# Optimization experiments

Measured on AMD Instinct MI355X. Metric: run time of the kernel, lower is better.

The kernel has to match this reference:

```python
import jax, jax.numpy as jnp
import numpy as np

B, H, S, D = 2, 16, 2048, 64
SCALE = D ** -0.5  # head_dim^-0.5 with dim=1024, num_heads=16


def setup_inputs() -> dict:
    key = jax.random.key(0)
    kq, kk, kv = jax.random.split(key, 3)
    q = jax.random.normal(kq, (B, H, S, D), dtype=jnp.float32)
    k = jax.random.normal(kk, (B, H, S, D), dtype=jnp.float32)
    v = jax.random.normal(kv, (B, H, S, D), dtype=jnp.float32)
    # causal mask, broadcastable over batch and heads; 0 -> masked
    mask = jnp.tril(jnp.ones((S, S), dtype=jnp.int32))[None, None]
    return {"q": q, "k": k, "v": v, "mask": mask}


def reference(q, k, v, mask):
    # scores: [B, H, S, S]
    scores = jnp.einsum("bhqd,bhkd->bhqk", q, k) * SCALE
    scores = jnp.where(mask == 0, jnp.float32(-jnp.inf), scores)
    attn_weights = jax.nn.softmax(scores, axis=-1)
    # dropout p=0 / eval mode -> identity
    attn_output = jnp.einsum("bhqk,bhkd->bhqd", attn_weights, v)
    return attn_output, attn_weights
```

## Files before the change

### kernel.cpp

```cpp
#include <hip/hip_runtime.h>


#define S_LEN 2048
#define HD 64
#define NHEADS 32
#define NQT 32
#define ATT_SCALE 0.125f

typedef __bf16 bf16x8 __attribute__((ext_vector_type(8)));
typedef unsigned short u16x8 __attribute__((ext_vector_type(8)));
typedef float f32x4 __attribute__((ext_vector_type(4)));

__device__ __forceinline__ unsigned short f2bf(float f) {
  unsigned int u = __builtin_bit_cast(unsigned int, f);
  u += 0x7fffu + ((u >> 16) & 1u);
  return (unsigned short)(u >> 16);
}
__device__ __forceinline__ bf16x8 frag16(const unsigned short* p) {
  uint4 u = *reinterpret_cast<const uint4*>(p);
  return __builtin_bit_cast(bf16x8, u);
}
__device__ __forceinline__ bf16x8 cvt8(const float* p) {
  const float4 a = *reinterpret_cast<const float4*>(p);
  const float4 b = *reinterpret_cast<const float4*>(p + 4);
  u16x8 r;
  r[0] = f2bf(a.x); r[1] = f2bf(a.y); r[2] = f2bf(a.z); r[3] = f2bf(a.w);
  r[4] = f2bf(b.x); r[5] = f2bf(b.y); r[6] = f2bf(b.z); r[7] = f2bf(b.w);
  return __builtin_bit_cast(bf16x8, r);
}
__device__ __forceinline__ bf16x8 load8(const void* base, size_t off, bool isf32) {
  if (isf32) return cvt8(reinterpret_cast<const float*>(base) + off);
  return frag16(reinterpret_cast<const unsigned short*>(base) + off);
}
__device__ __forceinline__ bool sniff_f32(const void* q) {
  const int lane = threadIdx.x & 63;
  const unsigned int w = reinterpret_cast<const unsigned int*>(q)[lane];
  const unsigned int le = (w >> 7) & 0xFFu;
  const bool okb = (le == 0u) || (le >= 100u && le <= 140u);
  return __popcll(__ballot(okb)) < 32;
}
__device__ __forceinline__ int swz3(int r) { return (r & 3) | (((r >> 3) & 1) << 2); }

__global__ __launch_bounds__(256) void prep_kernel(
    const void* __restrict__ q, const void* __restrict__ k, const void* __restrict__ v,
    unsigned short* __restrict__ wq, unsigned short* __restrict__ wk,
    unsigned short* __restrict__ wv) {
  __shared__ __align__(16) unsigned short T[HD][72];
  const int tid = threadIdx.x;
  if (blockIdx.x >= 1024) {
    const bool isf32 = sniff_f32(q);
    const size_t i = ((size_t)(blockIdx.x - 1024) * 256 + tid) * 8;
    bf16x8 a = load8(q, i, isf32);
    *reinterpret_cast<uint4*>(wq + i) = __builtin_bit_cast(uint4, a);
    bf16x8 b = load8(k, i, isf32);
    const int d0 = (int)(i & 63);
    const int t = (int)((i >> 6) & (S_LEN - 1));
    const int head = (int)(i >> 17);
    const int tl = t & 63;
    const int sch = (d0 >> 3) ^ swz3(tl);
    unsigned short* dst =
        wk + (((size_t)(head << 5) + (t >> 6)) << 12) + tl * 64 + (sch << 3);
    *reinterpret_cast<uint4*>(dst) = __builtin_bit_cast(uint4, b);
    return;
  }
  const bool isf32 = sniff_f32(v);
  const int head = blockIdx.x & (NHEADS - 1);
  const int tt = blockIdx.x >> 5;
  const int r = tid >> 2;
  const int dc = (tid & 3) << 4;
  const size_t off = ((size_t)head * S_LEN + (tt << 6) + r) * HD + dc;
  const bf16x8 x0 = load8(v, off, isf32);
  const bf16x8 x1 = load8(v, off + 8, isf32);
  const u16x8 e0 = __builtin_bit_cast(u16x8, x0);
  const u16x8 e1 = __builtin_bit_cast(u16x8, x1);
#pragma unroll
  for (int e = 0; e < 8; ++e) { T[dc + e][r] = e0[e]; T[dc + 8 + e][r] = e1[e]; }
  __syncthreads();
  const int d = tid >> 2;
  const int tc = (tid & 3) << 4;
  const int c0 = tc >> 3;
  unsigned short* base = wv + (((size_t)(head << 5) + tt) << 12) + d * 64;
  *reinterpret_cast<uint4*>(base + ((c0 ^ swz3(d)) << 3)) =
      *reinterpret_cast<const uint4*>(&T[d][tc]);
  *reinterpret_cast<uint4*>(base + (((c0 + 1) ^ swz3(d)) << 3)) =
      *reinterpret_cast<const uint4*>(&T[d][tc + 8]);
}

__global__ __launch_bounds__(256, 4) void attn_ws(
    const unsigned short* __restrict__ wq, const unsigned short* __restrict__ wk,
    const unsigned short* __restrict__ wv,
    float* __restrict__ out_o, float* __restrict__ out_w) {
  __shared__ __align__(16) unsigned short Kl[2][4096];
  __shared__ __align__(16) unsigned short Vl[2][4096];

  const int blk = blockIdx.x;
  const int head = blk & (NHEADS - 1);
  const int qt = (NQT - 1) - (blk >> 5);
  const int tid = threadIdx.x;
  const int lane = tid & 63;
  const int wave = tid >> 6;
  const int q0 = qt << 6;
  const int r0 = q0 + (wave << 4);
  const int l15 = lane & 15;
  const int quad = lane >> 4;
  const int kswz = (l15 & 3) | (((l15 >> 2) & 1) << 2);
  const int vswz = (l15 & 3) | (((l15 >> 3) & 1) << 2);
  const int krow_l = ((l15 >> 2) << 3) + (l15 & 3);
  const int qi = r0 + l15;

  float* Wh = out_w + (size_t)head * S_LEN * S_LEN;
  const unsigned short* wkh = wk + ((size_t)head << 17);
  const unsigned short* wvh = wv + ((size_t)head << 17);

  const size_t qoff = ((size_t)head << 17) + (size_t)(r0 + l15) * HD + (quad << 3);
  const bf16x8 qa0 = frag16(wq + qoff);
  const bf16x8 qa1 = frag16(wq + qoff + 32);

  const int so = wave * 1024 + lane * 8;
  uint4 sk0, sk1, sv0, sv1;
  auto ldKg = [&](int kt) {
    const unsigned short* p = wkh + ((size_t)kt << 12) + so;
    sk0 = *reinterpret_cast<const uint4*>(p);
    sk1 = *reinterpret_cast<const uint4*>(p + 512);
  };
  auto wrK = [&](int b) {
    unsigned short* p = &Kl[b][so];
    *reinterpret_cast<uint4*>(p) = sk0;
    *reinterpret_cast<uint4*>(p + 512) = sk1;
  };
  auto ldVg = [&](int kt) {
    const unsigned short* p = wvh + ((size_t)kt << 12) + so;
    sv0 = *reinterpret_cast<const uint4*>(p);
    sv1 = *reinterpret_cast<const uint4*>(p + 512);
  };
  auto wrV = [&](int b) {
    unsigned short* p = &Vl[b][so];
    *reinterpret_cast<uint4*>(p) = sv0;
    *reinterpret_cast<uint4*>(p + 512) = sv1;
  };

  float lsum = 0.f;
  ldKg(0); wrK(0); __syncthreads();
  for (int kt = 0; kt <= qt; ++kt) {
    if (kt < qt) ldKg(kt + 1);
    const unsigned short* Kb = &Kl[kt & 1][0];
#pragma unroll
    for (int s = 0; s < 4; ++s) {
      const int R = krow_l + ((s & 1) << 2) + ((s >> 1) << 5);
      const unsigned short* rb = Kb + R * 64;
      const bf16x8 k0 = frag16(rb + ((quad ^ kswz) << 3));
      const bf16x8 k1 = frag16(rb + (((4 + quad) ^ kswz) << 3));
      f32x4 acc = {0.f, 0.f, 0.f, 0.f};
      acc = __builtin_amdgcn_mfma_f32_16x16x32_bf16(k0, qa0, acc, 0, 0, 0);
      acc = __builtin_amdgcn_mfma_f32_16x16x32_bf16(k1, qa1, acc, 0, 0, 0);
      if (kt == qt) {
        const int kib = (kt << 6) + (quad << 3) + ((s & 1) << 2) + ((s >> 1) << 5);
#pragma unroll
        for (int r = 0; r < 4; ++r)
          lsum += (kib + r <= qi) ? __expf(acc[r] * ATT_SCALE) : 0.f;
      } else {
#pragma unroll
        for (int r = 0; r < 4; ++r) lsum += __expf(acc[r] * ATT_SCALE);
      }
    }
    if (kt < qt) { wrK((kt + 1) & 1); __syncthreads(); }
  }
  lsum += __shfl_xor(lsum, 16);
  lsum += __shfl_xor(lsum, 32);
  const float inv_l = 1.0f / lsum;
  __syncthreads();

  const f32x4 vz = {0.f, 0.f, 0.f, 0.f};
  f32x4 oacc[4] = {vz, vz, vz, vz};
  ldKg(0); ldVg(0); wrK(0); wrV(0); __syncthreads();
  for (int kt = 0; kt <= qt; ++kt) {
    const bool last = (kt == qt);
    if (!last) { ldKg(kt + 1); ldVg(kt + 1); }
    const unsigned short* Kb = &Kl[kt & 1][0];
    const unsigned short* Vb = &Vl[kt & 1][0];

    float pb[4][4];
#pragma unroll
    for (int s = 0; s < 4; ++s) {
      const int R = krow_l + ((s & 1) << 2) + ((s >> 1) << 5);
      const unsigned short* rb = Kb + R * 64;
      const bf16x8 k0 = frag16(rb + ((quad ^ kswz) << 3));
      const bf16x8 k1 = frag16(rb + (((4 + quad) ^ kswz) << 3));
      f32x4 acc = {0.f, 0.f, 0.f, 0.f};
      acc = __builtin_amdgcn_mfma_f32_16x16x32_bf16(k0, qa0, acc, 0, 0, 0);
      acc = __builtin_amdgcn_mfma_f32_16x16x32_bf16(k1, qa1, acc, 0, 0, 0);
      const int kib = (kt << 6) + (quad << 3) + ((s & 1) << 2) + ((s >> 1) << 5);
      f32x4 pv;
#pragma unroll
      for (int r = 0; r < 4; ++r) {
        float p = __expf(acc[r] * ATT_SCALE) * inv_l;
        if (last) p = (kib + r <= qi) ? p : 0.f;
        pb[s][r] = p;
        pv[r] = p;
      }
      *reinterpret_cast<f32x4*>(Wh + (size_t)qi * S_LEN + kib) = pv;
    }
    u16x8 a0, a1;
#pragma unroll
    for (int r = 0; r < 4; ++r) {
      a0[r] = f2bf(pb[0][r]); a0[4 + r] = f2bf(pb[1][r]);
      a1[r] = f2bf(pb[2][r]); a1[4 + r] = f2bf(pb[3][r]);
    }
    const bf16x8 pa0 = __builtin_bit_cast(bf16x8, a0);
    const bf16x8 pa1 = __builtin_bit_cast(bf16x8, a1);
#pragma unroll
    for (int nc2 = 0; nc2 < 4; ++nc2) {
      const unsigned short* rb = Vb + ((nc2 << 4) + l15) * 64;
      const bf16x8 v0 = frag16(rb + ((quad ^ vswz) << 3));
      const bf16x8 v1 = frag16(rb + (((4 + quad) ^ vswz) << 3));
      oacc[nc2] = __builtin_amdgcn_mfma_f32_16x16x32_bf16(pa0, v0, oacc[nc2], 0, 0, 0);
      oacc[nc2] = __builtin_amdgcn_mfma_f32_16x16x32_bf16(pa1, v1, oacc[nc2], 0, 0, 0);
    }
    if (!last) { wrK((kt + 1) & 1); wrV((kt + 1) & 1); __syncthreads(); }
  }

#pragma unroll
  for (int nc2 = 0; nc2 < 4; ++nc2)
#pragma unroll
    for (int r = 0; r < 4; ++r)
      out_o[(size_t)(head * S_LEN + r0 + (quad << 2) + r) * HD + (nc2 << 4) + l15] =
          oacc[nc2][r];

  {
    const int c0 = (qt + 1) << 6;
    const f32x4 z = {0.f, 0.f, 0.f, 0.f};
#pragma unroll 1
    for (int rr = 0; rr < 16; ++rr) {
      float* rowp = Wh + (size_t)(r0 + rr) * S_LEN;
      for (int c = c0 + (lane << 2); c < S_LEN; c += 256)
        __builtin_nontemporal_store(z, reinterpret_cast<f32x4*>(rowp + c));
    }
  }
}

__global__ __launch_bounds__(256, 4) void attn_fb(
    const void* __restrict__ q, const void* __restrict__ kk, const void* __restrict__ vv,
    float* __restrict__ out_o, float* __restrict__ out_w) {
  __shared__ __align__(16) unsigned short Vt[2 * HD * 72];

  const int blk = blockIdx.x;
  const int head = blk & (NHEADS - 1);
  const int qt = (NQT - 1) - (blk >> 5);
  const int tid = threadIdx.x;
  const int lane = tid & 63;
  const int wave = tid >> 6;
  const int q0 = qt << 6;
  const int r0 = q0 + (wave << 4);
  const int l15 = lane & 15;
  const int quad = lane >> 4;
  const bool isf32 = sniff_f32(q);

  const size_t qb = (size_t)head * S_LEN * HD;
  float* Wh = out_w + (size_t)head * S_LEN * S_LEN;

  {
    const int c0 = (qt + 1) << 6;
    const int nz4 = (S_LEN - c0) >> 2;
    const int row = tid >> 2;
    const f32x4 z = {0.f, 0.f, 0.f, 0.f};
    f32x4* wrow = reinterpret_cast<f32x4*>(Wh + (size_t)(q0 + row) * S_LEN + c0);
    for (int c = tid & 3; c < nz4; c += 4) wrow[c] = z;
  }

  const size_t qoff = qb + (size_t)(r0 + l15) * HD + (quad << 3);
  const bf16x8 qa0 = load8(q, qoff, isf32);
  const bf16x8 qa1 = load8(q, qoff + 32, isf32);

  const int krow_l = ((l15 >> 2) << 3) + (l15 & 3);
  auto ldk = [&](int kt, int f) -> bf16x8 {
    const int s = f >> 1;
    const int row = (kt << 6) + krow_l + ((s & 1) << 2) + ((s >> 1) << 5);
    const size_t o = qb + (size_t)row * HD + (quad << 3) + ((f & 1) << 5);
    return load8(kk, o, isf32);
  };
  const int kib_base = (quad << 3);
  const int qi = r0 + l15;

  float lsum = 0.f;
  {
    bf16x8 kc[8], kn[8];
#pragma unroll
    for (int f = 0; f < 8; ++f) kc[f] = ldk(0, f);
    for (int kt = 0; kt <= qt; ++kt) {
      if (kt < qt) {
#pragma unroll
        for (int f = 0; f < 8; ++f) kn[f] = ldk(kt + 1, f);
      }
#pragma unroll
      for (int s = 0; s < 4; ++s) {
        f32x4 acc = {0.f, 0.f, 0.f, 0.f};
        acc = __builtin_amdgcn_mfma_f32_16x16x32_bf16(kc[2 * s], qa0, acc, 0, 0, 0);
        acc = __builtin_amdgcn_mfma_f32_16x16x32_bf16(kc[2 * s + 1], qa1, acc, 0, 0, 0);
        const int kib = (kt << 6) + kib_base + ((s & 1) << 2) + ((s >> 1) << 5);
#pragma unroll
        for (int r = 0; r < 4; ++r)
          lsum += (kt < qt || kib + r <= qi) ? __expf(acc[r] * ATT_SCALE) : 0.f;
      }
      if (kt < qt) {
#pragma unroll
        for (int f = 0; f < 8; ++f) kc[f] = kn[f];
      }
    }
  }
  lsum += __shfl_xor(lsum, 16);
  lsum += __shfl_xor(lsum, 32);
  const float inv_l = 1.0f / lsum;

  const f32x4 vz = {0.f, 0.f, 0.f, 0.f};
  f32x4 oacc[4] = {vz, vz, vz, vz};

  const int ftr1 = tid >> 3, fdc = (tid & 7) << 3;
  const int ftr2 = (tid + 256) >> 3;
  bf16x8 fv0, fv1;
  auto vload = [&](int kt) {
    fv0 = load8(vv, qb + (size_t)((kt << 6) + ftr1) * HD + fdc, isf32);
    fv1 = load8(vv, qb + (size_t)((kt << 6) + ftr2) * HD + fdc, isf32);
  };
  auto vstage = [&](int buf) {
    const u16x8 s0 = __builtin_bit_cast(u16x8, fv0);
    const u16x8 s1 = __builtin_bit_cast(u16x8, fv1);
    const int tb1 = ftr1 >> 3, tl1 = ftr1 & 7;
    const int tb2 = ftr2 >> 3, tl2 = ftr2 & 7;
    unsigned short* Vb = &Vt[buf * HD * 72];
#pragma unroll
    for (int e = 0; e < 8; ++e) {
      const int d = fdc + e;
      Vb[d * 72 + (((tb1 ^ (d >> 3)) << 3) | tl1)] = s0[e];
      Vb[d * 72 + (((tb2 ^ (d >> 3)) << 3) | tl2)] = s1[e];
    }
  };
  vload(0);
  vstage(0);
  __syncthreads();
  for (int kt = 0; kt <= qt; ++kt) {
    const bool last = (kt == qt);
    bf16x8 kf[8];
#pragma unroll
    for (int f = 0; f < 8; ++f) kf[f] = ldk(kt, f);
    if (!last) vload(kt + 1);

    float pb[4][4];
#pragma unroll
    for (int s = 0; s < 4; ++s) {
      f32x4 acc = {0.f, 0.f, 0.f, 0.f};
      acc = __builtin_amdgcn_mfma_f32_16x16x32_bf16(kf[2 * s], qa0, acc, 0, 0, 0);
      acc = __builtin_amdgcn_mfma_f32_16x16x32_bf16(kf[2 * s + 1], qa1, acc, 0, 0, 0);
      const int kib = (kt << 6) + kib_base + ((s & 1) << 2) + ((s >> 1) << 5);
      f32x4 pv;
#pragma unroll
      for (int r = 0; r < 4; ++r) {
        float p = __expf(acc[r] * ATT_SCALE) * inv_l;
        if (last) p = (kib + r <= qi) ? p : 0.f;
        pb[s][r] = p;
        pv[r] = p;
      }
      *reinterpret_cast<f32x4*>(Wh + (size_t)qi * S_LEN + kib) = pv;
    }
    u16x8 a0, a1;
#pragma unroll
    for (int r = 0; r < 4; ++r) {
      a0[r] = f2bf(pb[0][r]); a0[4 + r] = f2bf(pb[1][r]);
      a1[r] = f2bf(pb[2][r]); a1[4 + r] = f2bf(pb[3][r]);
    }
    const bf16x8 pa0 = __builtin_bit_cast(bf16x8, a0);
    const bf16x8 pa1 = __builtin_bit_cast(bf16x8, a1);
    const unsigned short* Vc = &Vt[(kt & 1) * HD * 72];
#pragma unroll
    for (int nc2 = 0; nc2 < 4; ++nc2) {
      const int n = (nc2 << 4) + l15;
      const unsigned short* vbp = Vc + n * 72;
      const int nb = n >> 3;
      const bf16x8 v0 = frag16(vbp + ((quad ^ nb) << 3));
      const bf16x8 v1 = frag16(vbp + (((4 + quad) ^ nb) << 3));
      oacc[nc2] = __builtin_amdgcn_mfma_f32_16x16x32_bf16(pa0, v0, oacc[nc2], 0, 0, 0);
      oacc[nc2] = __builtin_amdgcn_mfma_f32_16x16x32_bf16(pa1, v1, oacc[nc2], 0, 0, 0);
    }
    if (!last) {
      vstage((kt + 1) & 1);
      __syncthreads();
    }
  }

#pragma unroll
  for (int nc2 = 0; nc2 < 4; ++nc2)
#pragma unroll
    for (int r = 0; r < 4; ++r)
      out_o[(size_t)(head * S_LEN + r0 + (quad << 2) + r) * HD + (nc2 << 4) + l15] =
          oacc[nc2][r];
}

extern "C" void kernel_launch(void* const* d_in, const int* in_sizes, int n_in,
                              void* d_out, int out_size, void* d_ws, size_t ws_size,
                              hipStream_t stream) {
  (void)in_sizes; (void)n_in; (void)out_size;
  const void* q = d_in[0];
  const void* k = d_in[1];
  const void* v = d_in[2];
  float* out = (float*)d_out;
  float* out_o = out;
  float* out_w = out + (size_t)NHEADS * S_LEN * HD;
  const size_t NE = (size_t)NHEADS * S_LEN * HD;
  if (d_ws && ws_size >= NE * 2 * 3) {
    unsigned short* wq = reinterpret_cast<unsigned short*>(d_ws);
    unsigned short* wk = wq + NE;
    unsigned short* wv = wk + NE;
    prep_kernel<<<dim3(1024 + NE / (256 * 8)), dim3(256), 0, stream>>>(q, k, v, wq, wk, wv);
    attn_ws<<<dim3(NHEADS * NQT), dim3(256), 0, stream>>>(wq, wk, wv, out_o, out_w);
  } else {
    attn_fb<<<dim3(NHEADS * NQT), dim3(256), 0, stream>>>(q, k, v, out_o, out_w);
  }
}
```

Measured before the change: 634.4 us.

## Double query rows per block, pair causal tiles, and map heads to XCDs

Each block now handles 128 query rows, with each wave computing two 16-row groups, so every K/V tile loaded into shared memory serves twice as many rows. The grid is cut to 512 blocks. Block indices are remapped so each XCD handles four heads, which keeps K/V reads for a head within one L2. Query tiles are ordered so long and short causal tiles are interleaved to balance load. The costs are more registers (launch bounds lowered to 2 blocks per SIMD), fewer blocks in flight, and some wasted work on the masked half of the diagonal tiles.

```diff
diff --git a/kernel.cpp b/kernel.cpp
--- a/kernel.cpp
+++ b/kernel.cpp
@@ -86,35 +86,44 @@
       *reinterpret_cast<const uint4*>(&T[d][tc + 8]);
 }
 
-__global__ __launch_bounds__(256, 4) void attn_ws(
+__global__ __launch_bounds__(256, 2) void attn_ws(
     const unsigned short* __restrict__ wq, const unsigned short* __restrict__ wk,
     const unsigned short* __restrict__ wv,
     float* __restrict__ out_o, float* __restrict__ out_w) {
   __shared__ __align__(16) unsigned short Kl[2][4096];
   __shared__ __align__(16) unsigned short Vl[2][4096];
 
-  const int blk = blockIdx.x;
-  const int head = blk & (NHEADS - 1);
-  const int qt = (NQT - 1) - (blk >> 5);
+  const int b = blockIdx.x;
+  const int xcd = b & 7;
+  const int slot = b >> 3;
+  const int head = (xcd << 2) + (slot & 3);
+  const int u = slot >> 2;
+  const int jj = (u < 8) ? u : (23 - u);
+  const int qthi = 2 * jj + 1;
+  const int q0 = jj << 7;
+
   const int tid = threadIdx.x;
   const int lane = tid & 63;
   const int wave = tid >> 6;
-  const int q0 = qt << 6;
-  const int r0 = q0 + (wave << 4);
   const int l15 = lane & 15;
   const int quad = lane >> 4;
   const int kswz = (l15 & 3) | (((l15 >> 2) & 1) << 2);
   const int vswz = (l15 & 3) | (((l15 >> 3) & 1) << 2);
   const int krow_l = ((l15 >> 2) << 3) + (l15 & 3);
-  const int qi = r0 + l15;
+  const int rg0 = q0 + (wave << 5);
+  const int rg1 = rg0 + 16;
+  const int qi0 = rg0 + l15;
+  const int qi1 = rg1 + l15;
 
   float* Wh = out_w + (size_t)head * S_LEN * S_LEN;
   const unsigned short* wkh = wk + ((size_t)head << 17);
   const unsigned short* wvh = wv + ((size_t)head << 17);
 
-  const size_t qoff = ((size_t)head << 17) + (size_t)(r0 + l15) * HD + (quad << 3);
-  const bf16x8 qa0 = frag16(wq + qoff);
-  const bf16x8 qa1 = frag16(wq + qoff + 32);
+  const size_t hq = (size_t)head << 17;
+  const bf16x8 qa00 = frag16(wq + hq + (size_t)qi0 * HD + (quad << 3));
+  const bf16x8 qa01 = frag16(wq + hq + (size_t)qi0 * HD + (quad << 3) + 32);
+  const bf16x8 qa10 = frag16(wq + hq + (size_t)qi1 * HD + (quad << 3));
+  const bf16x8 qa11 = frag16(wq + hq + (size_t)qi1 * HD + (quad << 3) + 32);
 
   const int so = wave * 1024 + lane * 8;
   uint4 sk0, sk1, sv0, sv1;
@@ -123,8 +132,8 @@
     sk0 = *reinterpret_cast<const uint4*>(p);
     sk1 = *reinterpret_cast<const uint4*>(p + 512);
   };
-  auto wrK = [&](int b) {
-    unsigned short* p = &Kl[b][so];
+  auto wrK = [&](int bb) {
+    unsigned short* p = &Kl[bb][so];
     *reinterpret_cast<uint4*>(p) = sk0;
     *reinterpret_cast<uint4*>(p + 512) = sk1;
   };
@@ -133,88 +142,122 @@
     sv0 = *reinterpret_cast<const uint4*>(p);
     sv1 = *reinterpret_cast<const uint4*>(p + 512);
   };
-  auto wrV = [&](int b) {
-    unsigned short* p = &Vl[b][so];
+  auto wrV = [&](int bb) {
+    unsigned short* p = &Vl[bb][so];
     *reinterpret_cast<uint4*>(p) = sv0;
     *reinterpret_cast<uint4*>(p + 512) = sv1;
   };
 
-  float lsum = 0.f;
+  float ls0 = 0.f, ls1 = 0.f;
   ldKg(0); wrK(0); __syncthreads();
-  for (int kt = 0; kt <= qt; ++kt) {
-    if (kt < qt) ldKg(kt + 1);
+  for (int kt = 0; kt <= qthi; ++kt) {
+    if (kt < qthi) ldKg(kt + 1);
     const unsigned short* Kb = &Kl[kt & 1][0];
+    const int kb6 = kt << 6;
+    const bool m0 = kb6 + 63 > rg0;
+    const bool m1 = kb6 + 63 > rg1;
 #pragma unroll
     for (int s = 0; s < 4; ++s) {
       const int R = krow_l + ((s & 1) << 2) + ((s >> 1) << 5);
       const unsigned short* rb = Kb + R * 64;
       const bf16x8 k0 = frag16(rb + ((quad ^ kswz) << 3));
       const bf16x8 k1 = frag16(rb + (((4 + quad) ^ kswz) << 3));
-      f32x4 acc = {0.f, 0.f, 0.f, 0.f};
-      acc = __builtin_amdgcn_mfma_f32_16x16x32_bf16(k0, qa0, acc, 0, 0, 0);
-      acc = __builtin_amdgcn_mfma_f32_16x16x32_bf16(k1, qa1, acc, 0, 0, 0);
-      if (kt == qt) {
-        const int kib = (kt << 6) + (quad << 3) + ((s & 1) << 2) + ((s >> 1) << 5);
+      const int kib = kb6 + (quad << 3) + ((s & 1) << 2) + ((s >> 1) << 5);
+      f32x4 a0 = {0.f, 0.f, 0.f, 0.f};
+      a0 = __builtin_amdgcn_mfma_f32_16x16x32_bf16(k0, qa00, a0, 0, 0, 0);
+      a0 = __builtin_amdgcn_mfma_f32_16x16x32_bf16(k1, qa01, a0, 0, 0, 0);
+      f32x4 a1 = {0.f, 0.f, 0.f, 0.f};
+      a1 = __builtin_amdgcn_mfma_f32_16x16x32_bf16(k0, qa10, a1, 0, 0, 0);
+      a1 = __builtin_amdgcn_mfma_f32_16x16x32_bf16(k1, qa11, a1, 0, 0, 0);
+      if (m0) {
 #pragma unroll
         for (int r = 0; r < 4; ++r)
-          lsum += (kib + r <= qi) ? __expf(acc[r] * ATT_SCALE) : 0.f;
+          ls0 += (kib + r <= qi0) ? __expf(a0[r] * ATT_SCALE) : 0.f;
       } else {
 #pragma unroll
-        for (int r = 0; r < 4; ++r) lsum += __expf(acc[r] * ATT_SCALE);
-      }
-    }
-    if (kt < qt) { wrK((kt + 1) & 1); __syncthreads(); }
-  }
-  lsum += __shfl_xor(lsum, 16);
-  lsum += __shfl_xor(lsum, 32);
-  const float inv_l = 1.0f / lsum;
+        for (int r = 0; r < 4; ++r) ls0 += __expf(a0[r] * ATT_SCALE);
+      }
+      if (m1) {
+#pragma unroll
+        for (int r = 0; r < 4; ++r)
+          ls1 += (kib + r <= qi1) ? __expf(a1[r] * ATT_SCALE) : 0.f;
+      } else {
+#pragma unroll
+        for (int r = 0; r < 4; ++r) ls1 += __expf(a1[r] * ATT_SCALE);
+      }
+    }
+    if (kt < qthi) { wrK((kt + 1) & 1); __syncthreads(); }
+  }
+  ls0 += __shfl_xor(ls0, 16); ls0 += __shfl_xor(ls0, 32);
+  ls1 += __shfl_xor(ls1, 16); ls1 += __shfl_xor(ls1, 32);
+  const float inv_l0 = 1.0f / ls0;
+  const float inv_l1 = 1.0f / ls1;
   __syncthreads();
 
   const f32x4 vz = {0.f, 0.f, 0.f, 0.f};
-  f32x4 oacc[4] = {vz, vz, vz, vz};
+  f32x4 o0[4] = {vz, vz, vz, vz};
+  f32x4 o1[4] = {vz, vz, vz, vz};
   ldKg(0); ldVg(0); wrK(0); wrV(0); __syncthreads();
-  for (int kt = 0; kt <= qt; ++kt) {
-    const bool last = (kt == qt);
+  for (int kt = 0; kt <= qthi; ++kt) {
+    const bool last = (kt == qthi);
     if (!last) { ldKg(kt + 1); ldVg(kt + 1); }
     const unsigned short* Kb = &Kl[kt & 1][0];
     const unsigned short* Vb = &Vl[kt & 1][0];
-
-    float pb[4][4];
+    const int kb6 = kt << 6;
+    const bool m0 = kb6 + 63 > rg0;
+    const bool m1 = kb6 + 63 > rg1;
+
+    float pb0[4][4], pb1[4][4];
 #pragma unroll
     for (int s = 0; s < 4; ++s) {
       const int R = krow_l + ((s & 1) << 2) + ((s >> 1) << 5);
       const unsigned short* rb = Kb + R * 64;
       const bf16x8 k0 = frag16(rb + ((quad ^ kswz) << 3));
       const bf16x8 k1 = frag16(rb + (((4 + quad) ^ kswz) << 3));
-      f32x4 acc = {0.f, 0.f, 0.f, 0.f};
-      acc = __builtin_amdgcn_mfma_f32_16x16x32_bf16(k0, qa0, acc, 0, 0, 0);
-      acc = __builtin_amdgcn_mfma_f32_16x16x32_bf16(k1, qa1, acc, 0, 0, 0);
-      const int kib = (kt << 6) + (quad << 3) + ((s & 1) << 2) + ((s >> 1) << 5);
-      f32x4 pv;
+      const int kib = kb6 + (quad << 3) + ((s & 1) << 2) + ((s >> 1) << 5);
+      f32x4 a0 = {0.f, 0.f, 0.f, 0.f};
+      a0 = __builtin_amdgcn_mfma_f32_16x16x32_bf16(k0, qa00, a0, 0, 0, 0);
+      a0 = __builtin_amdgcn_mfma_f32_16x16x32_bf16(k1, qa01, a0, 0, 0, 0);
+      f32x4 a1 = {0.f, 0.f, 0.f, 0.f};
+      a1 = __builtin_amdgcn_mfma_f32_16x16x32_bf16(k0, qa10, a1, 0, 0, 0);
+      a1 = __builtin_amdgcn_mfma_f32_16x16x32_bf16(k1, qa11, a1, 0, 0, 0);
+      f32x4 p0, p1;
 #pragma unroll
       for (int r = 0; r < 4; ++r) {
-        float p = __expf(acc[r] * ATT_SCALE) * inv_l;
-        if (last) p = (kib + r <= qi) ? p : 0.f;
-        pb[s][r] = p;
-        pv[r] = p;
-      }
-      *reinterpret_cast<f32x4*>(Wh + (size_t)qi * S_LEN + kib) = pv;
-    }
-    u16x8 a0, a1;
+        float p = __expf(a0[r] * ATT_SCALE) * inv_l0;
+        if (m0) p = (kib + r <= qi0) ? p : 0.f;
+        pb0[s][r] = p; p0[r] = p;
+      }
+#pragma unroll
+      for (int r = 0; r < 4; ++r) {
+        float p = __expf(a1[r] * ATT_SCALE) * inv_l1;
+        if (m1) p = (kib + r <= qi1) ? p : 0.f;
+        pb1[s][r] = p; p1[r] = p;
+      }
+      *reinterpret_cast<f32x4*>(Wh + (size_t)qi0 * S_LEN + kib) = p0;
+      *reinterpret_cast<f32x4*>(Wh + (size_t)qi1 * S_LEN + kib) = p1;
+    }
+    u16x8 c00, c01, c10, c11;
 #pragma unroll
     for (int r = 0; r < 4; ++r) {
-      a0[r] = f2bf(pb[0][r]); a0[4 + r] = f2bf(pb[1][r]);
-      a1[r] = f2bf(pb[2][r]); a1[4 + r] = f2bf(pb[3][r]);
-    }
-    const bf16x8 pa0 = __builtin_bit_cast(bf16x8, a0);
-    const bf16x8 pa1 = __builtin_bit_cast(bf16x8, a1);
+      c00[r] = f2bf(pb0[0][r]); c00[4 + r] = f2bf(pb0[1][r]);
+      c01[r] = f2bf(pb0[2][r]); c01[4 + r] = f2bf(pb0[3][r]);
+      c10[r] = f2bf(pb1[0][r]); c10[4 + r] = f2bf(pb1[1][r]);
+      c11[r] = f2bf(pb1[2][r]); c11[4 + r] = f2bf(pb1[3][r]);
+    }
+    const bf16x8 pa00 = __builtin_bit_cast(bf16x8, c00);
+    const bf16x8 pa01 = __builtin_bit_cast(bf16x8, c01);
+    const bf16x8 pa10 = __builtin_bit_cast(bf16x8, c10);
+    const bf16x8 pa11 = __builtin_bit_cast(bf16x8, c11);
 #pragma unroll
     for (int nc2 = 0; nc2 < 4; ++nc2) {
       const unsigned short* rb = Vb + ((nc2 << 4) + l15) * 64;
       const bf16x8 v0 = frag16(rb + ((quad ^ vswz) << 3));
       const bf16x8 v1 = frag16(rb + (((4 + quad) ^ vswz) << 3));
-      oacc[nc2] = __builtin_amdgcn_mfma_f32_16x16x32_bf16(pa0, v0, oacc[nc2], 0, 0, 0);
-      oacc[nc2] = __builtin_amdgcn_mfma_f32_16x16x32_bf16(pa1, v1, oacc[nc2], 0, 0, 0);
+      o0[nc2] = __builtin_amdgcn_mfma_f32_16x16x32_bf16(pa00, v0, o0[nc2], 0, 0, 0);
+      o0[nc2] = __builtin_amdgcn_mfma_f32_16x16x32_bf16(pa01, v1, o0[nc2], 0, 0, 0);
+      o1[nc2] = __builtin_amdgcn_mfma_f32_16x16x32_bf16(pa10, v0, o1[nc2], 0, 0, 0);
+      o1[nc2] = __builtin_amdgcn_mfma_f32_16x16x32_bf16(pa11, v1, o1[nc2], 0, 0, 0);
     }
     if (!last) { wrK((kt + 1) & 1); wrV((kt + 1) & 1); __syncthreads(); }
   }
@@ -222,16 +265,19 @@
 #pragma unroll
   for (int nc2 = 0; nc2 < 4; ++nc2)
 #pragma unroll
-    for (int r = 0; r < 4; ++r)
-      out_o[(size_t)(head * S_LEN + r0 + (quad << 2) + r) * HD + (nc2 << 4) + l15] =
-          oacc[nc2][r];
+    for (int r = 0; r < 4; ++r) {
+      out_o[(size_t)(head * S_LEN + rg0 + (quad << 2) + r) * HD + (nc2 << 4) + l15] =
+          o0[nc2][r];
+      out_o[(size_t)(head * S_LEN + rg1 + (quad << 2) + r) * HD + (nc2 << 4) + l15] =
+          o1[nc2][r];
+    }
 
   {
-    const int c0 = (qt + 1) << 6;
+    const int c0 = q0 + 128;
     const f32x4 z = {0.f, 0.f, 0.f, 0.f};
 #pragma unroll 1
-    for (int rr = 0; rr < 16; ++rr) {
-      float* rowp = Wh + (size_t)(r0 + rr) * S_LEN;
+    for (int rr = 0; rr < 32; ++rr) {
+      float* rowp = Wh + (size_t)(rg0 + rr) * S_LEN;
       for (int c = c0 + (lane << 2); c < S_LEN; c += 256)
         __builtin_nontemporal_store(z, reinterpret_cast<f32x4*>(rowp + c));
     }
@@ -410,7 +456,7 @@
     unsigned short* wk = wq + NE;
     unsigned short* wv = wk + NE;
     prep_kernel<<<dim3(1024 + NE / (256 * 8)), dim3(256), 0, stream>>>(q, k, v, wq, wk, wv);
-    attn_ws<<<dim3(NHEADS * NQT), dim3(256), 0, stream>>>(wq, wk, wv, out_o, out_w);
+    attn_ws<<<dim3(512), dim3(256), 0, stream>>>(wq, wk, wv, out_o, out_w);
   } else {
     attn_fb<<<dim3(NHEADS * NQT), dim3(256), 0, stream>>>(q, k, v, out_o, out_w);
   }
```

After: 648.2 us. +2.2%, slower.

## Process two K tiles per barrier in sum pass, add MFMA priority and nontemporal stores

Applied to the files above, without the earlier changes.

The first (row-sum) pass now stages two K tiles per iteration in a four-buffer shared array, halving the number of barriers and issuing two global loads ahead. MFMA sections are wrapped in s_setprio to favor matrix issue across waves. The attention-weight and output stores become nontemporal to avoid polluting cache with write-only data. The cost is more registers for the prefetch and somewhat more complex loop control.

```diff
diff --git a/kernel.cpp b/kernel.cpp
--- a/kernel.cpp
+++ b/kernel.cpp
@@ -90,8 +90,7 @@
     const unsigned short* __restrict__ wq, const unsigned short* __restrict__ wk,
     const unsigned short* __restrict__ wv,
     float* __restrict__ out_o, float* __restrict__ out_w) {
-  __shared__ __align__(16) unsigned short Kl[2][4096];
-  __shared__ __align__(16) unsigned short Vl[2][4096];
+  __shared__ __align__(16) unsigned short Tl[4][4096];
 
   const int blk = blockIdx.x;
   const int head = blk & (NHEADS - 1);
@@ -117,33 +116,20 @@
   const bf16x8 qa1 = frag16(wq + qoff + 32);
 
   const int so = wave * 1024 + lane * 8;
-  uint4 sk0, sk1, sv0, sv1;
-  auto ldKg = [&](int kt) {
-    const unsigned short* p = wkh + ((size_t)kt << 12) + so;
-    sk0 = *reinterpret_cast<const uint4*>(p);
-    sk1 = *reinterpret_cast<const uint4*>(p + 512);
-  };
-  auto wrK = [&](int b) {
-    unsigned short* p = &Kl[b][so];
-    *reinterpret_cast<uint4*>(p) = sk0;
-    *reinterpret_cast<uint4*>(p + 512) = sk1;
-  };
-  auto ldVg = [&](int kt) {
-    const unsigned short* p = wvh + ((size_t)kt << 12) + so;
-    sv0 = *reinterpret_cast<const uint4*>(p);
-    sv1 = *reinterpret_cast<const uint4*>(p + 512);
-  };
-  auto wrV = [&](int b) {
-    unsigned short* p = &Vl[b][so];
-    *reinterpret_cast<uint4*>(p) = sv0;
-    *reinterpret_cast<uint4*>(p + 512) = sv1;
+  auto gload = [&](const unsigned short* src, int kt, uint4& x0, uint4& x1) {
+    const unsigned short* p = src + ((size_t)kt << 12) + so;
+    x0 = *reinterpret_cast<const uint4*>(p);
+    x1 = *reinterpret_cast<const uint4*>(p + 512);
+  };
+  auto lwrite = [&](int buf, const uint4& x0, const uint4& x1) {
+    unsigned short* p = &Tl[buf][so];
+    *reinterpret_cast<uint4*>(p) = x0;
+    *reinterpret_cast<uint4*>(p + 512) = x1;
   };
 
   float lsum = 0.f;
-  ldKg(0); wrK(0); __syncthreads();
-  for (int kt = 0; kt <= qt; ++kt) {
-    if (kt < qt) ldKg(kt + 1);
-    const unsigned short* Kb = &Kl[kt & 1][0];
+  auto qk_sum = [&](int kt, int buf) {
+    const unsigned short* Kb = &Tl[buf][0];
 #pragma unroll
     for (int s = 0; s < 4; ++s) {
       const int R = krow_l + ((s & 1) << 2) + ((s >> 1) << 5);
@@ -151,8 +137,10 @@
       const bf16x8 k0 = frag16(rb + ((quad ^ kswz) << 3));
       const bf16x8 k1 = frag16(rb + (((4 + quad) ^ kswz) << 3));
       f32x4 acc = {0.f, 0.f, 0.f, 0.f};
+      __builtin_amdgcn_s_setprio(1);
       acc = __builtin_amdgcn_mfma_f32_16x16x32_bf16(k0, qa0, acc, 0, 0, 0);
       acc = __builtin_amdgcn_mfma_f32_16x16x32_bf16(k1, qa1, acc, 0, 0, 0);
+      __builtin_amdgcn_s_setprio(0);
       if (kt == qt) {
         const int kib = (kt << 6) + (quad << 3) + ((s & 1) << 2) + ((s >> 1) << 5);
 #pragma unroll
@@ -163,7 +151,29 @@
         for (int r = 0; r < 4; ++r) lsum += __expf(acc[r] * ATT_SCALE);
       }
     }
-    if (kt < qt) { wrK((kt + 1) & 1); __syncthreads(); }
+  };
+  {
+    const int ntiles = qt + 1;
+    uint4 a0, a1, b0, b1;
+    gload(wkh, 0, a0, a1); lwrite(0, a0, a1);
+    if (ntiles > 1) { gload(wkh, 1, b0, b1); lwrite(1, b0, b1); }
+    __syncthreads();
+#pragma unroll 1
+    for (int g = 0;; ++g) {
+      const int t0 = 2 * g;
+      const bool lastg = (t0 + 2 >= ntiles);
+      if (!lastg) {
+        gload(wkh, t0 + 2, a0, a1);
+        if (t0 + 3 < ntiles) gload(wkh, t0 + 3, b0, b1);
+      }
+      qk_sum(t0, (g & 1) << 1);
+      if (t0 + 1 < ntiles) qk_sum(t0 + 1, ((g & 1) << 1) + 1);
+      if (lastg) break;
+      const int nb = ((g + 1) & 1) << 1;
+      lwrite(nb, a0, a1);
+      if (t0 + 3 < ntiles) lwrite(nb + 1, b0, b1);
+      __syncthreads();
+    }
   }
   lsum += __shfl_xor(lsum, 16);
   lsum += __shfl_xor(lsum, 32);
@@ -172,59 +182,75 @@
 
   const f32x4 vz = {0.f, 0.f, 0.f, 0.f};
   f32x4 oacc[4] = {vz, vz, vz, vz};
-  ldKg(0); ldVg(0); wrK(0); wrV(0); __syncthreads();
-  for (int kt = 0; kt <= qt; ++kt) {
-    const bool last = (kt == qt);
-    if (!last) { ldKg(kt + 1); ldVg(kt + 1); }
-    const unsigned short* Kb = &Kl[kt & 1][0];
-    const unsigned short* Vb = &Vl[kt & 1][0];
-
-    float pb[4][4];
-#pragma unroll
-    for (int s = 0; s < 4; ++s) {
-      const int R = krow_l + ((s & 1) << 2) + ((s >> 1) << 5);
-      const unsigned short* rb = Kb + R * 64;
-      const bf16x8 k0 = frag16(rb + ((quad ^ kswz) << 3));
-      const bf16x8 k1 = frag16(rb + (((4 + quad) ^ kswz) << 3));
-      f32x4 acc = {0.f, 0.f, 0.f, 0.f};
-      acc = __builtin_amdgcn_mfma_f32_16x16x32_bf16(k0, qa0, acc, 0, 0, 0);
-      acc = __builtin_amdgcn_mfma_f32_16x16x32_bf16(k1, qa1, acc, 0, 0, 0);
-      const int kib = (kt << 6) + (quad << 3) + ((s & 1) << 2) + ((s >> 1) << 5);
-      f32x4 pv;
+  {
+    uint4 ka0, ka1, va0, va1;
+    gload(wkh, 0, ka0, ka1); gload(wvh, 0, va0, va1);
+    lwrite(0, ka0, ka1); lwrite(2, va0, va1);
+    __syncthreads();
+#pragma unroll 1
+    for (int kt = 0; kt <= qt; ++kt) {
+      const bool last = (kt == qt);
+      if (!last) { gload(wkh, kt + 1, ka0, ka1); gload(wvh, kt + 1, va0, va1); }
+      const unsigned short* Kb = &Tl[kt & 1][0];
+      const unsigned short* Vb = &Tl[2 + (kt & 1)][0];
+
+      float pb[4][4];
+#pragma unroll
+      for (int s = 0; s < 4; ++s) {
+        const int R = krow_l + ((s & 1) << 2) + ((s >> 1) << 5);
+        const unsigned short* rb = Kb + R * 64;
+        const bf16x8 k0 = frag16(rb + ((quad ^ kswz) << 3));
+        const bf16x8 k1 = frag16(rb + (((4 + quad) ^ kswz) << 3));
+        f32x4 acc = {0.f, 0.f, 0.f, 0.f};
+        __builtin_amdgcn_s_setprio(1);
+        acc = __builtin_amdgcn_mfma_f32_16x16x32_bf16(k0, qa0, acc, 0, 0, 0);
+        acc = __builtin_amdgcn_mfma_f32_16x16x32_bf16(k1, qa1, acc, 0, 0, 0);
+        __builtin_amdgcn_s_setprio(0);
+        const int kib = (kt << 6) + (quad << 3) + ((s & 1) << 2) + ((s >> 1) << 5);
+        f32x4 pv;
+#pragma unroll
+        for (int r = 0; r < 4; ++r) {
+          float p = __expf(acc[r] * ATT_SCALE) * inv_l;
+          if (last) p = (kib + r <= qi) ? p : 0.f;
+          pb[s][r] = p;
+          pv[r] = p;
+        }
+        __builtin_nontemporal_store(
+            pv, reinterpret_cast<f32x4*>(Wh + (size_t)qi * S_LEN + kib));
+      }
+      u16x8 a0, a1;
 #pragma unroll
       for (int r = 0; r < 4; ++r) {
-        float p = __expf(acc[r] * ATT_SCALE) * inv_l;
-        if (last) p = (kib + r <= qi) ? p : 0.f;
-        pb[s][r] = p;
-        pv[r] = p;
-      }
-      *reinterpret_cast<f32x4*>(Wh + (size_t)qi * S_LEN + kib) = pv;
-    }
-    u16x8 a0, a1;
-#pragma unroll
-    for (int r = 0; r < 4; ++r) {
-      a0[r] = f2bf(pb[0][r]); a0[4 + r] = f2bf(pb[1][r]);
-      a1[r] = f2bf(pb[2][r]); a1[4 + r] = f2bf(pb[3][r]);
-    }
-    const bf16x8 pa0 = __builtin_bit_cast(bf16x8, a0);
-    const bf16x8 pa1 = __builtin_bit_cast(bf16x8, a1);
-#pragma unroll
-    for (int nc2 = 0; nc2 < 4; ++nc2) {
-      const unsigned short* rb = Vb + ((nc2 << 4) + l15) * 64;
-      const bf16x8 v0 = frag16(rb + ((quad ^ vswz) << 3));
-      const bf16x8 v1 = frag16(rb + (((4 + quad) ^ vswz) << 3));
-      oacc[nc2] = __builtin_amdgcn_mfma_f32_16x16x32_bf16(pa0, v0, oacc[nc2], 0, 0, 0);
-      oacc[nc2] = __builtin_amdgcn_mfma_f32_16x16x32_bf16(pa1, v1, oacc[nc2], 0, 0, 0);
-    }
-    if (!last) { wrK((kt + 1) & 1); wrV((kt + 1) & 1); __syncthreads(); }
+        a0[r] = f2bf(pb[0][r]); a0[4 + r] = f2bf(pb[1][r]);
+        a1[r] = f2bf(pb[2][r]); a1[4 + r] = f2bf(pb[3][r]);
+      }
+      const bf16x8 pa0 = __builtin_bit_cast(bf16x8, a0);
+      const bf16x8 pa1 = __builtin_bit_cast(bf16x8, a1);
+      __builtin_amdgcn_s_setprio(1);
+#pragma unroll
+      for (int nc2 = 0; nc2 < 4; ++nc2) {
+        const unsigned short* rb = Vb + ((nc2 << 4) + l15) * 64;
+        const bf16x8 v0 = frag16(rb + ((quad ^ vswz) << 3));
+        const bf16x8 v1 = frag16(rb + (((4 + quad) ^ vswz) << 3));
+        oacc[nc2] = __builtin_amdgcn_mfma_f32_16x16x32_bf16(pa0, v0, oacc[nc2], 0, 0, 0);
+        oacc[nc2] = __builtin_amdgcn_mfma_f32_16x16x32_bf16(pa1, v1, oacc[nc2], 0, 0, 0);
+      }
+      __builtin_amdgcn_s_setprio(0);
+      if (!last) {
+        lwrite((kt + 1) & 1, ka0, ka1);
+        lwrite(2 + ((kt + 1) & 1), va0, va1);
+        __syncthreads();
+      }
+    }
   }
 
 #pragma unroll
   for (int nc2 = 0; nc2 < 4; ++nc2)
 #pragma unroll
     for (int r = 0; r < 4; ++r)
-      out_o[(size_t)(head * S_LEN + r0 + (quad << 2) + r) * HD + (nc2 << 4) + l15] =
-          oacc[nc2][r];
+      __builtin_nontemporal_store(
+          oacc[nc2][r],
+          out_o + (size_t)(head * S_LEN + r0 + (quad << 2) + r) * HD + (nc2 << 4) + l15);
 
   {
     const int c0 = (qt + 1) << 6;
```

After: 762.6 us. 20.2% more time.
